# Optimization experiments

Hardware: AMD Instinct MI355X
Metric: run time of the kernel (lower is better)

The kernel has to match this reference:

```python
import jax, jax.numpy as jnp
import numpy as np

INPUT_DIM = 4096
EPS = 1e-8


def _ste_bit(v):
    # {0,1} bit with straight-through gradient
    b = (v >= 0).astype(v.dtype)
    return v + jax.lax.stop_gradient(b - v)


def _ste_sign(v):
    # {-1,+1} sign with straight-through gradient
    s = jnp.where(v >= 0, 1.0, -1.0).astype(v.dtype)
    return v + jax.lax.stop_gradient(s - v)


def setup_inputs() -> dict:
    key = jax.random.key(0)
    k1, k2, k3 = jax.random.split(key, 3)
    x = jax.random.normal(k1, (8192, 4096), dtype=jnp.float32)
    mag_bits = jax.random.normal(k2, (3, 4096, 4096), dtype=jnp.float32)  # [nbBits-1, in, out]
    sign_bit = jax.random.normal(k3, (4096, 4096), dtype=jnp.float32)     # [in, out]
    return {"x": x, "mag_bits": mag_bits, "sign_bit": sign_bit}


def reference(x, mag_bits, sign_bit):
    nbits = mag_bits.shape[0]
    # bit-plane composition: W_mag = sum_k bit_k * 2^-(k+1)
    powers = (2.0 ** -(jnp.arange(1, nbits + 1))).astype(mag_bits.dtype)  # [K]
    bits = _ste_bit(mag_bits)                                             # [K, in, out]
    w = _ste_sign(sign_bit) * jnp.einsum('kio,k->io', bits, powers)       # [in, out]
    # rescale so std(W) matches kaiming std (original does this via a detached
    # numpy round-trip, so no gradient flows through alpha)
    std_target = np.sqrt(2.0 / INPUT_DIM).astype(np.float32)
    alpha = jax.lax.stop_gradient(std_target / (jnp.std(w) + EPS))
    w = w * alpha
    # F.linear(x, W.T) == x @ W
    return x @ w
```

## Files before the change

kernel.cpp:

```cpp
#include <hip/hip_runtime.h>
#include <hip/hip_bf16.h>
#include <stdint.h>

#define K_DIM 4096
#define M_DIM 8192
#define N_DIM 4096

typedef short bf16x8 __attribute__((ext_vector_type(8)));
typedef float f32x4  __attribute__((ext_vector_type(4)));

__device__ __forceinline__ uint16_t f2bf(float f) {
  uint32_t u = __float_as_uint(f);
  u += 0x7fffu + ((u >> 16) & 1u);
  return (uint16_t)(u >> 16);
}

__device__ __forceinline__ float wval(float b0, float b1, float b2, float sg) {
  float mg = (b0 >= 0.f ? 0.5f : 0.f) + (b1 >= 0.f ? 0.25f : 0.f) + (b2 >= 0.f ? 0.125f : 0.f);
  return (sg >= 0.f) ? mg : -mg;
}

__device__ __forceinline__ void gload16(const void* g, void* l) {
  typedef __attribute__((address_space(1))) const uint32_t gu32;
  typedef __attribute__((address_space(3))) uint32_t lu32;
  __builtin_amdgcn_global_load_lds((gu32*)g, (lu32*)l, 16, 0, 0);
}

__global__ __launch_bounds__(256) void build_wt(
    const float* __restrict__ mag, const float* __restrict__ sgn,
    uint16_t* __restrict__ wt, float* __restrict__ psum, float* __restrict__ psumsq)
{
  __shared__ float wl[64][65];
  __shared__ float parts[8];
  const int tid = threadIdx.x;
  const int lr = tid >> 4;
  const int lc = tid & 15;
  const int i0 = blockIdx.y * 64;
  const int o0 = blockIdx.x * 64;
  const float* m0 = mag;
  const float* m1 = mag + (size_t)K_DIM * N_DIM;
  const float* m2 = mag + 2 * (size_t)K_DIM * N_DIM;

  float s = 0.f, s2 = 0.f;
  #pragma unroll
  for (int rg = 0; rg < 4; ++rg) {
    int il = rg * 16 + lr;
    size_t base = (size_t)(i0 + il) * N_DIM + o0 + lc * 4;
    float4 a = *(const float4*)(m0 + base);
    float4 b = *(const float4*)(m1 + base);
    float4 c = *(const float4*)(m2 + base);
    float4 g = *(const float4*)(sgn + base);
    float w0 = wval(a.x, b.x, c.x, g.x);
    float w1 = wval(a.y, b.y, c.y, g.y);
    float w2 = wval(a.z, b.z, c.z, g.z);
    float w3 = wval(a.w, b.w, c.w, g.w);
    wl[il][lc * 4 + 0] = w0;
    wl[il][lc * 4 + 1] = w1;
    wl[il][lc * 4 + 2] = w2;
    wl[il][lc * 4 + 3] = w3;
    s  += w0 + w1 + w2 + w3;
    s2 += w0 * w0 + w1 * w1 + w2 * w2 + w3 * w3;
  }
  #pragma unroll
  for (int off = 32; off > 0; off >>= 1) {
    s  += __shfl_down(s,  off);
    s2 += __shfl_down(s2, off);
  }
  if ((tid & 63) == 0) { parts[tid >> 6] = s; parts[4 + (tid >> 6)] = s2; }
  __syncthreads();
  if (tid == 0) {
    int bid = blockIdx.y * gridDim.x + blockIdx.x;
    psum[bid]   = parts[0] + parts[1] + parts[2] + parts[3];
    psumsq[bid] = parts[4] + parts[5] + parts[6] + parts[7];
  }
  #pragma unroll
  for (int rg = 0; rg < 4; ++rg) {
    int ol = rg * 16 + lr;
    int il = lc * 4;
    ushort4 v;
    v.x = f2bf(wl[il + 0][ol]);
    v.y = f2bf(wl[il + 1][ol]);
    v.z = f2bf(wl[il + 2][ol]);
    v.w = f2bf(wl[il + 3][ol]);
    *(ushort4*)(wt + (size_t)(o0 + ol) * K_DIM + i0 + il) = v;
  }
}

__global__ __launch_bounds__(256) void cvt_x(const float* __restrict__ x,
                                             uint16_t* __restrict__ xb, int n8)
{
  int idx = blockIdx.x * blockDim.x + threadIdx.x;
  int stride = gridDim.x * blockDim.x;
  for (; idx < n8; idx += stride) {
    float4 v0 = ((const float4*)x)[2 * idx];
    float4 v1 = ((const float4*)x)[2 * idx + 1];
    ushort4 r0, r1;
    r0.x = f2bf(v0.x); r0.y = f2bf(v0.y); r0.z = f2bf(v0.z); r0.w = f2bf(v0.w);
    r1.x = f2bf(v1.x); r1.y = f2bf(v1.y); r1.z = f2bf(v1.z); r1.w = f2bf(v1.w);
    ((ushort4*)xb)[2 * idx]     = r0;
    ((ushort4*)xb)[2 * idx + 1] = r1;
  }
}

__global__ __launch_bounds__(256) void calc_alpha(const float* __restrict__ psum,
                                                  const float* __restrict__ psumsq,
                                                  float* __restrict__ alpha, int nparts)
{
  __shared__ float ls[256], lq[256];
  int tid = threadIdx.x;
  float s = 0.f, q = 0.f;
  for (int i = tid; i < nparts; i += 256) { s += psum[i]; q += psumsq[i]; }
  ls[tid] = s; lq[tid] = q;
  __syncthreads();
  for (int off = 128; off > 0; off >>= 1) {
    if (tid < off) { ls[tid] += ls[tid + off]; lq[tid] += lq[tid + off]; }
    __syncthreads();
  }
  if (tid == 0) {
    const float n = 16777216.f;
    float mean = ls[0] / n;
    float var  = lq[0] / n - mean * mean;
    var = var < 0.f ? 0.f : var;
    float stdv = sqrtf(var);
    alpha[0] = 0.022097086912079608f / (stdv + 1e-8f);
  }
}

#define NKT 64

__global__ __launch_bounds__(512, 2) void gemm_bf16_pl(
    const uint16_t* __restrict__ xb, const uint16_t* __restrict__ wt,
    const float* __restrict__ alphap, float* __restrict__ out)
{
  __shared__ __align__(16) unsigned char sA[2][256 * 128];
  __shared__ __align__(16) unsigned char sB[2][256 * 128];

  const int tid  = threadIdx.x;
  const int lane = tid & 63;
  const int wv   = tid >> 6;
  const int wm   = wv >> 2;
  const int wn   = wv & 3;

  const int bid = blockIdx.x;
  const int xcd = bid & 7;
  const int c   = bid >> 3;
  const int bm  = (xcd >> 1) * 8 + (c >> 3);
  const int bn  = (xcd & 1) * 8 + (c & 7);

  const size_t rowA0 = (size_t)bm * 256;
  const size_t rowB0 = (size_t)bn * 256;

  f32x4 acc[8][4] = {};

  const int l15   = lane & 15;
  const int src_x = ((lane & 7) ^ (lane >> 3)) << 4;
  const int cb0   = (((lane >> 4) << 4)) ^ ((lane & 7) << 4);
  const int cb1   = (64 | ((lane >> 4) << 4)) ^ ((lane & 7) << 4);

#define STA(cc, mh, h, kt)                                                          \
  gload16((const char*)xb + (((rowA0 + (h) * 128 + (mh) * 64 + wv * 8 + (lane >> 3)) \
              * (size_t)K_DIM + (size_t)(kt) * 64) << 1) + src_x,                   \
          &sA[cc][((mh) * 128 + (h) * 64 + wv * 8) * 128])
#define STB(cc, bh, h, kt)                                                          \
  gload16((const char*)wt + (((rowB0 + (2 * (h) + (wv >> 2)) * 64 + (bh) * 32       \
              + (wv & 3) * 8 + (lane >> 3)) * (size_t)K_DIM + (size_t)(kt) * 64) << 1) + src_x, \
          &sB[cc][((bh) * 128 + (h) * 64 + wv * 8) * 128])
#define STAGE_TILE(cc, kt) do {                                                     \
    STA(cc, 0, 0, kt); STA(cc, 0, 1, kt); STA(cc, 1, 0, kt); STA(cc, 1, 1, kt);     \
    STB(cc, 0, 0, kt); STB(cc, 0, 1, kt); STB(cc, 1, 0, kt); STB(cc, 1, 1, kt);     \
  } while (0)

#define LDA8(Ap, mh, dst) do { _Pragma("unroll")                                    \
  for (int m = 0; m < 4; ++m) {                                                     \
    const unsigned char* rp = (Ap) + (size_t)((mh) * 128 + wm * 64 + m * 16 + l15) * 128; \
    dst[2 * m]     = *(const bf16x8*)(rp + cb0);                                    \
    dst[2 * m + 1] = *(const bf16x8*)(rp + cb1); } } while (0)
#define LDB4(Bp, bh, dst) do { _Pragma("unroll")                                    \
  for (int n = 0; n < 2; ++n) {                                                     \
    const unsigned char* rp = (Bp) + (size_t)((bh) * 128 + wn * 32 + n * 16 + l15) * 128; \
    dst[2 * n]     = *(const bf16x8*)(rp + cb0);                                    \
    dst[2 * n + 1] = *(const bf16x8*)(rp + cb1); } } while (0)

#define MMQ(AF, BF, mh, bh) do {                                                    \
  __builtin_amdgcn_s_setprio(1);                                                    \
  _Pragma("unroll") for (int m = 0; m < 4; ++m)                                     \
    _Pragma("unroll") for (int n = 0; n < 2; ++n) {                                 \
      acc[(mh)*4+m][(bh)*2+n] = __builtin_amdgcn_mfma_f32_16x16x32_bf16(            \
          AF[2*m],   BF[2*n],   acc[(mh)*4+m][(bh)*2+n], 0, 0, 0);                  \
      acc[(mh)*4+m][(bh)*2+n] = __builtin_amdgcn_mfma_f32_16x16x32_bf16(            \
          AF[2*m+1], BF[2*n+1], acc[(mh)*4+m][(bh)*2+n], 0, 0, 0); }                \
  __builtin_amdgcn_s_setprio(0); } while (0)

#define SCHED0   __builtin_amdgcn_sched_barrier(0)
#define LGKMC(N) do { asm volatile("s_waitcnt lgkmcnt(" #N ")" ::: "memory"); SCHED0; } while (0)
#define WAITV(N) do { asm volatile("s_waitcnt vmcnt(" #N ")"   ::: "memory"); SCHED0; } while (0)
#define BAR      do { asm volatile("s_barrier" ::: "memory"); SCHED0; } while (0)

  bf16x8 A0f[8], A1f[8], B0f[4], B1f[4];

  STAGE_TILE(0, 0);
  STAGE_TILE(1, 1);
  WAITV(8); BAR;
  {
    const unsigned char* Ap = sA[0];
    const unsigned char* Bp = sB[0];
    LDA8(Ap, 0, A0f); LDB4(Bp, 0, B0f); SCHED0;
  }

  #pragma unroll 1
  for (int u = 0; u < NKT; ++u) {
    const unsigned char* Ap = sA[u & 1];
    const unsigned char* Bp = sB[u & 1];
    const unsigned char* An = sA[(u + 1) & 1];
    const unsigned char* Bn = sB[(u + 1) & 1];

    LDB4(Bp, 1, B1f); SCHED0;
    LDA8(Ap, 1, A1f); SCHED0;

    LGKMC(12);
    MMQ(A0f, B0f, 0, 0);
    LGKMC(8);
    MMQ(A0f, B1f, 0, 1);
    LGKMC(0);
    WAITV(0);
    BAR;

    if (u + 2 < NKT) { STAGE_TILE(u & 1, u + 2); SCHED0; }

    MMQ(A1f, B0f, 1, 0);

    if (u + 1 < NKT) {
      LDA8(An, 0, A0f); LDB4(Bn, 0, B0f); SCHED0;
    }

    MMQ(A1f, B1f, 1, 1);
    SCHED0;
  }

#undef STA
#undef STB
#undef STAGE_TILE
#undef LDA8
#undef LDB4
#undef MMQ
#undef SCHED0
#undef LGKMC
#undef WAITV
#undef BAR

  const float alpha = alphap[0];
  const int ccol  = bn * 256 + wn * 64 + l15;
  const int crow0 = bm * 256 + wm * 128 + ((lane >> 4) << 2);
  #pragma unroll
  for (int am = 0; am < 8; ++am)
    #pragma unroll
    for (int an = 0; an < 4; ++an)
      #pragma unroll
      for (int r = 0; r < 4; ++r)
        out[(size_t)(crow0 + am * 16 + r) * N_DIM + ccol + an * 16] = acc[am][an][r] * alpha;
}

extern "C" void kernel_launch(void* const* d_in, const int* in_sizes, int n_in,
                              void* d_out, int out_size, void* d_ws, size_t ws_size,
                              hipStream_t stream) {
  const float* x   = (const float*)d_in[0];
  const float* mag = (const float*)d_in[1];
  const float* sgn = (const float*)d_in[2];
  float* out = (float*)d_out;

  char* ws = (char*)d_ws;
  float* alpha    = (float*)ws;
  float* psum     = (float*)(ws + 256);
  float* psumsq   = (float*)(ws + 256 + 16384);
  uint16_t* wt    = (uint16_t*)(ws + 256 + 32768);
  uint16_t* xb    = (uint16_t*)(ws + 256 + 32768 + 33554432ull);
  size_t needed = 256 + 32768 + 33554432ull + 67108864ull;
  if (ws_size < needed) return;

  build_wt<<<dim3(64, 64), 256, 0, stream>>>(mag, sgn, wt, psum, psumsq);
  cvt_x<<<dim3(2048), 256, 0, stream>>>(x, xb, (M_DIM * K_DIM) / 8);
  calc_alpha<<<dim3(1), 256, 0, stream>>>(psum, psumsq, alpha, 4096);
  gemm_bf16_pl<<<dim3(512), 512, 0, stream>>>(xb, wt, alpha, out);
}
```

Before: 351.6 us.

## Split GEMM main loop into four interleaved stage/load/MFMA phases per K-tile

Restructures the bf16 GEMM mainloop so each K-tile is split into four phases. Each phase issues one quarter of the next tile's global-to-LDS copies, waits with a partial vmcnt, reads one fragment set from LDS and runs one quarter of the MFMAs. The aim is to spread global loads and LDS reads evenly across the MFMA work instead of bunching them around one barrier. In exchange it adds more barriers and full lgkmcnt waits per tile. The last two iterations also redundantly reload tile 63 into the buffers.

```diff
diff --git a/kernel.cpp b/kernel.cpp
--- a/kernel.cpp
+++ b/kernel.cpp
@@ -126,9 +126,7 @@
   }
 }
 
-#define NKT 64
-
-__global__ __launch_bounds__(512, 2) void gemm_bf16_pl(
+__global__ __launch_bounds__(512, 2) void gemm_bf16_u4(
     const uint16_t* __restrict__ xb, const uint16_t* __restrict__ wt,
     const float* __restrict__ alphap, float* __restrict__ out)
 {
@@ -165,10 +163,8 @@
   gload16((const char*)wt + (((rowB0 + (2 * (h) + (wv >> 2)) * 64 + (bh) * 32       \
               + (wv & 3) * 8 + (lane >> 3)) * (size_t)K_DIM + (size_t)(kt) * 64) << 1) + src_x, \
           &sB[cc][((bh) * 128 + (h) * 64 + wv * 8) * 128])
-#define STAGE_TILE(cc, kt) do {                                                     \
-    STA(cc, 0, 0, kt); STA(cc, 0, 1, kt); STA(cc, 1, 0, kt); STA(cc, 1, 1, kt);     \
-    STB(cc, 0, 0, kt); STB(cc, 0, 1, kt); STB(cc, 1, 0, kt); STB(cc, 1, 1, kt);     \
-  } while (0)
+#define STAGE_A(cc, mh, kt) do { STA(cc, mh, 0, kt); STA(cc, mh, 1, kt); } while (0)
+#define STAGE_B(cc, bh, kt) do { STB(cc, bh, 0, kt); STB(cc, bh, 1, kt); } while (0)
 
 #define LDA8(Ap, mh, dst) do { _Pragma("unroll")                                    \
   for (int m = 0; m < 4; ++m) {                                                     \
@@ -192,59 +188,62 @@
   __builtin_amdgcn_s_setprio(0); } while (0)
 
 #define SCHED0   __builtin_amdgcn_sched_barrier(0)
-#define LGKMC(N) do { asm volatile("s_waitcnt lgkmcnt(" #N ")" ::: "memory"); SCHED0; } while (0)
+#define LGKM0    do { asm volatile("s_waitcnt lgkmcnt(0)" ::: "memory"); SCHED0; } while (0)
 #define WAITV(N) do { asm volatile("s_waitcnt vmcnt(" #N ")"   ::: "memory"); SCHED0; } while (0)
 #define BAR      do { asm volatile("s_barrier" ::: "memory"); SCHED0; } while (0)
 
   bf16x8 A0f[8], A1f[8], B0f[4], B1f[4];
 
-  STAGE_TILE(0, 0);
-  STAGE_TILE(1, 1);
-  WAITV(8); BAR;
-  {
-    const unsigned char* Ap = sA[0];
-    const unsigned char* Bp = sB[0];
-    LDA8(Ap, 0, A0f); LDB4(Bp, 0, B0f); SCHED0;
-  }
+  STAGE_A(0, 0, 0); STAGE_B(0, 0, 0); STAGE_B(0, 1, 0); STAGE_A(0, 1, 0);
+  STAGE_A(1, 0, 1); STAGE_B(1, 0, 1);
+  WAITV(8);
+  BAR;
+  LDA8(sA[0], 0, A0f); LDB4(sB[0], 0, B0f); SCHED0;
+  STAGE_B(1, 1, 1); STAGE_A(1, 1, 1);
 
   #pragma unroll 1
-  for (int u = 0; u < NKT; ++u) {
-    const unsigned char* Ap = sA[u & 1];
-    const unsigned char* Bp = sB[u & 1];
-    const unsigned char* An = sA[(u + 1) & 1];
-    const unsigned char* Bn = sB[(u + 1) & 1];
-
-    LDB4(Bp, 1, B1f); SCHED0;
-    LDA8(Ap, 1, A1f); SCHED0;
-
-    LGKMC(12);
-    MMQ(A0f, B0f, 0, 0);
-    LGKMC(8);
-    MMQ(A0f, B1f, 0, 1);
-    LGKMC(0);
-    WAITV(0);
-    BAR;
-
-    if (u + 2 < NKT) { STAGE_TILE(u & 1, u + 2); SCHED0; }
-
-    MMQ(A1f, B0f, 1, 0);
-
-    if (u + 1 < NKT) {
-      LDA8(An, 0, A0f); LDB4(Bn, 0, B0f); SCHED0;
-    }
-
-    MMQ(A1f, B1f, 1, 1);
-    SCHED0;
+  for (int u = 0; u < 64; ++u) {
+    const int cc = u & 1, oc = cc ^ 1;
+    const unsigned char* Acur = sA[cc];
+    const unsigned char* Bcur = sB[cc];
+    const unsigned char* Aoth = sA[oc];
+    const unsigned char* Both = sB[oc];
+    const int k2 = (u + 2 < 64) ? (u + 2) : 63;
+
+    STAGE_A(cc, 0, k2);
+    WAITV(12); BAR; LGKM0;
+    LDB4(Bcur, 1, B1f); SCHED0;
+    MMQ(A0f, B0f, 0, 0); SCHED0;
+    BAR;
+
+    STAGE_B(cc, 0, k2);
+    WAITV(12); BAR; LGKM0;
+    LDA8(Acur, 1, A1f); SCHED0;
+    MMQ(A0f, B1f, 0, 1); SCHED0;
+    BAR;
+
+    STAGE_B(cc, 1, k2);
+    WAITV(12); BAR; LGKM0;
+    LDA8(Aoth, 0, A0f); SCHED0;
+    MMQ(A1f, B0f, 1, 0); SCHED0;
+    BAR;
+
+    STAGE_A(cc, 1, k2);
+    WAITV(12); BAR; LGKM0;
+    LDB4(Both, 0, B0f); SCHED0;
+    MMQ(A1f, B1f, 1, 1); SCHED0;
+    BAR;
   }
 
 #undef STA
 #undef STB
-#undef STAGE_TILE
+#undef STAGE_A
+#undef STAGE_B
 #undef LDA8
 #undef LDB4
 #undef MMQ
 #undef SCHED0
-#undef LGKMC
+#undef LGKM0
 #undef WAITV
 #undef BAR
 
@@ -280,5 +279,5 @@
   build_wt<<<dim3(64, 64), 256, 0, stream>>>(mag, sgn, wt, psum, psumsq);
   cvt_x<<<dim3(2048), 256, 0, stream>>>(x, xb, (M_DIM * K_DIM) / 8);
   calc_alpha<<<dim3(1), 256, 0, stream>>>(psum, psumsq, alpha, 4096);
-  gemm_bf16_pl<<<dim3(512), 512, 0, stream>>>(xb, wt, alpha, out);
-}
+  gemm_bf16_u4<<<dim3(512), 512, 0, stream>>>(xb, wt, alpha, out);
+}
```

Result: slower. 404.5 us (+15.0%).
